# Kernel tuning notes

Measured on AMD Instinct MI355X. Metric: run time of the kernel, lower is better.

Reference implementation:

```python
import jax, jax.numpy as jnp
import numpy as np
import math

D_MODEL = 1024
N_HEADS = 16
HEAD_DIM = D_MODEL // N_HEADS


def rotate_half(x):
    x1, x2 = x[..., : x.shape[-1] // 2], x[..., x.shape[-1] // 2 :]
    return jnp.concatenate([-x2, x1], axis=-1)


def rope_cos_sin(T, dim, dtype):
    inv_freq = 1.0 / (10000.0 ** (jnp.arange(0, dim, 2, dtype=jnp.float32) / dim))
    t = jnp.arange(T, dtype=jnp.float32)
    freqs = jnp.einsum('i,j->ij', t, inv_freq)          # [T, dim/2]
    emb = jnp.concatenate([freqs, freqs], axis=-1)      # [T, dim]
    # broadcast shape [1, T, 1, dim] to match q/k of shape [B, T, H, dim]
    return emb.astype(dtype)[None, :, None, :]


def setup_inputs() -> dict:
    key = jax.random.key(0)
    k_x, k_qkv_w, k_qkv_b, k_p_w, k_p_b = jax.random.split(key, 5)
    B, T = 2, 2048
    s = 1.0 / math.sqrt(D_MODEL)
    return {
        'x': jax.random.normal(k_x, (B, T, D_MODEL), dtype=jnp.float32),
        'qkv_w': jax.random.uniform(k_qkv_w, (3 * D_MODEL, D_MODEL), minval=-s, maxval=s, dtype=jnp.float32),
        'qkv_b': jax.random.uniform(k_qkv_b, (3 * D_MODEL,), minval=-s, maxval=s, dtype=jnp.float32),
        'proj_w': jax.random.uniform(k_p_w, (D_MODEL, D_MODEL), minval=-s, maxval=s, dtype=jnp.float32),
        'proj_b': jax.random.uniform(k_p_b, (D_MODEL,), minval=-s, maxval=s, dtype=jnp.float32),
    }


def reference(x, qkv_w, qkv_b, proj_w, proj_b):
    B, T, C = x.shape
    H, Dh = N_HEADS, HEAD_DIM
    qkv = x @ qkv_w.T + qkv_b                           # [B, T, 3C]
    qkv = qkv.reshape(B, T, 3, H, Dh)
    q, k, v = qkv[:, :, 0], qkv[:, :, 1], qkv[:, :, 2]  # [B, T, H, Dh]
    emb = rope_cos_sin(T, Dh, x.dtype)
    cos, sin = jnp.cos(emb), jnp.sin(emb)
    q = q * cos + rotate_half(q) * sin
    k = k * cos + rotate_half(k) * sin
    # attention with causal mask (dropout in eval mode = identity)
    scale = 1.0 / math.sqrt(Dh)
    attn = jnp.einsum('bqhd,bkhd->bhqk', q, k) * scale  # [B, H, T, T]
    causal = jnp.tril(jnp.ones((T, T), dtype=bool))
    attn = jnp.where(causal, attn, -jnp.inf)
    attn = jax.nn.softmax(attn, axis=-1)
    out = jnp.einsum('bhqk,bkhd->bqhd', attn, v).reshape(B, T, C)
    return out @ proj_w.T + proj_b
```

## Files before the change

### kernel.cpp

```cpp
#include <hip/hip_runtime.h>
#include <math.h>

#define T_SEQ 2048
#define NB 2
#define NH 16
#define DH 64
#define DM 1024

typedef unsigned short u16;
typedef __attribute__((ext_vector_type(8))) __bf16 bf16x8;
typedef __attribute__((ext_vector_type(4))) __bf16 bf16v4;
typedef __attribute__((ext_vector_type(4))) short s16x4;
typedef __attribute__((ext_vector_type(4))) float f32x4;
typedef __attribute__((ext_vector_type(4))) int i32x4;

__device__ __forceinline__ u16 f2bf(float f) {
  return __builtin_bit_cast(u16, (__bf16)f);
}
__device__ __forceinline__ float bf2f(u16 v) {
  unsigned u = ((unsigned)v) << 16;
  return __builtin_bit_cast(float, u);
}
__device__ __forceinline__ bf16x8 ld_frag(const u16* p) {
  bf16x8 r; __builtin_memcpy(&r, p, 16); return r;
}
__device__ __forceinline__ s16x4 ld8(const u16* p) {
  s16x4 r; __builtin_memcpy(&r, p, 8); return r;
}
__device__ __forceinline__ i32x4 ld16(const u16* p) {
  i32x4 r; __builtin_memcpy(&r, p, 16); return r;
}
__device__ __forceinline__ void st16(u16* p, i32x4 v) {
  __builtin_memcpy(p, &v, 16);
}
__device__ __forceinline__ void cvt_store8(u16* dst, const float* src) {
  f32x4 a, b;
  __builtin_memcpy(&a, src, 16);
  __builtin_memcpy(&b, src + 4, 16);
  bf16x8 t;
  t[0] = (__bf16)a[0]; t[1] = (__bf16)a[1]; t[2] = (__bf16)a[2]; t[3] = (__bf16)a[3];
  t[4] = (__bf16)b[0]; t[5] = (__bf16)b[1]; t[6] = (__bf16)b[2]; t[7] = (__bf16)b[3];
  __builtin_memcpy(dst, &t, 16);
}
__device__ __forceinline__ void gld_lds16(const u16* g, u16* l) {
  __builtin_amdgcn_global_load_lds(
      (const __attribute__((address_space(1))) void*)g,
      (__attribute__((address_space(3))) void*)l, 16, 0, 0);
}

__global__ __launch_bounds__(256) void cvt_f32_bf16(const float* __restrict__ in,
                                                    u16* __restrict__ out, int n8) {
  const int i = blockIdx.x * 256 + threadIdx.x;
  if (i < n8) cvt_store8(out + (long)i * 8, in + (long)i * 8);
}

template <int MODE, int BN>
__global__ __launch_bounds__(256) void gemm_nt(
    const u16* __restrict__ A, const u16* __restrict__ Bw,
    const float* __restrict__ bias, float* __restrict__ out,
    u16* __restrict__ q_ws, u16* __restrict__ k_ws, u16* __restrict__ v_ws,
    int M, int N, int K) {
  constexpr int NTN = BN / 32;
  constexpr int WNS = BN / 2;
  __shared__ __align__(16) u16 As[128 * 32];
  __shared__ __align__(16) u16 Bs[BN * 32];
  const int tid = threadIdx.x;
  const int wave = tid >> 6, lane = tid & 63;
  const int quad = lane >> 4, l16 = lane & 15;
  const int wm = wave & 1, wn = wave >> 1;
  const int m0 = blockIdx.y * 128, n0 = blockIdx.x * BN;
  const int lrow = lane >> 2;
  const int lcol = (lane & 3) * 8;

  f32x4 acc[4][NTN] = {};

  const u16* Ag = A + (long)(m0 + wave * 16 + lrow) * K + lcol;
  const u16* Bg = Bw + (long)(n0 + wave * 16 + lrow) * K + lcol;
  u16* Al = &As[(wave * 16 + lrow) * 32 + lcol];
  u16* Bl = &Bs[(wave * 16 + lrow) * 32 + lcol];

  for (int k0 = 0; k0 < K; k0 += 32) {
    __syncthreads();
    gld_lds16(Ag + k0, Al);
    gld_lds16(Ag + (long)64 * K + k0, Al + 64 * 32);
    gld_lds16(Bg + k0, Bl);
    if constexpr (BN == 128) gld_lds16(Bg + (long)64 * K + k0, Bl + 64 * 32);
    __syncthreads();
    bf16x8 af[4], bfr[NTN];
#pragma unroll
    for (int mt = 0; mt < 4; mt++)
      af[mt] = ld_frag(&As[(wm * 64 + mt * 16 + l16) * 32 + quad * 8]);
#pragma unroll
    for (int nt = 0; nt < NTN; nt++)
      bfr[nt] = ld_frag(&Bs[(wn * WNS + nt * 16 + l16) * 32 + quad * 8]);
#pragma unroll
    for (int mt = 0; mt < 4; mt++)
#pragma unroll
      for (int nt = 0; nt < NTN; nt++)
        acc[mt][nt] = __builtin_amdgcn_mfma_f32_16x16x32_bf16(af[mt], bfr[nt],
                                                              acc[mt][nt], 0, 0, 0);
  }

  if constexpr (MODE == 1) {
#pragma unroll
    for (int nt = 0; nt < NTN; nt++) {
      const int col = n0 + wn * WNS + nt * 16 + l16;
      const float bv = bias[col];
#pragma unroll
      for (int mt = 0; mt < 4; mt++) {
        const int rbase = m0 + wm * 64 + mt * 16 + quad * 4;
#pragma unroll
        for (int r = 0; r < 4; r++)
          out[(long)(rbase + r) * N + col] = acc[mt][nt][r] + bv;
      }
    }
  } else {
    const int which = n0 >> 10;
#pragma unroll
    for (int np = 0; np < 2; np++) {
      const int col1 = n0 + wn * 64 + np * 16 + l16;
      const int rem = col1 & 1023;
      const int h = rem >> 6, dh = rem & 63;
      const float bv1 = bias[col1], bv2 = bias[col1 + 32];
      if (which == 2) {
#pragma unroll
        for (int mt = 0; mt < 4; mt++) {
          const int rbase = m0 + wm * 64 + mt * 16 + quad * 4;
          const int b = rbase >> 11;
#pragma unroll
          for (int r = 0; r < 4; r++) {
            const int t = (rbase + r) & (T_SEQ - 1);
            const long vb = (((long)(b * NH + h)) * DH) * T_SEQ + t;
            v_ws[vb + (long)dh * T_SEQ] = f2bf(acc[mt][np][r] + bv1);
            v_ws[vb + (long)(dh + 32) * T_SEQ] = f2bf(acc[mt][np + 2][r] + bv2);
          }
        }
      } else {
        const float invf = exp2f(-(float)dh * 0.41524101186092045f);
        const float cD = cosf(invf), sD = sinf(invf);
        u16* dst = (which == 0) ? q_ws : k_ws;
        const float sc = (which == 0) ? 0.125f : 1.0f;
#pragma unroll
        for (int mt = 0; mt < 4; mt++) {
          const int rbase = m0 + wm * 64 + mt * 16 + quad * 4;
          const int b = rbase >> 11;
          const int t0 = rbase & (T_SEQ - 1);
          float c = cosf((float)t0 * invf), s = sinf((float)t0 * invf);
#pragma unroll
          for (int r = 0; r < 4; r++) {
            const float v1 = acc[mt][np][r] + bv1;
            const float v2 = acc[mt][np + 2][r] + bv2;
            const float o1 = (v1 * c - v2 * s) * sc;
            const float o2 = (v2 * c + v1 * s) * sc;
            const long ib = (((long)(b * NH + h)) * T_SEQ + (t0 + r)) * DH;
            dst[ib + dh] = f2bf(o1);
            dst[ib + dh + 32] = f2bf(o2);
            const float cn = c * cD - s * sD;
            s = s * cD + c * sD;
            c = cn;
          }
        }
      }
    }
  }
}

__global__ __launch_bounds__(256, 4) void attn_kernel(const u16* __restrict__ q,
                                                      const u16* __restrict__ k,
                                                      const u16* __restrict__ v,
                                                      u16* __restrict__ o) {
  __shared__ __align__(16) u16 Ks[128 * 72];
  __shared__ __align__(16) u16 Vt[64 * 136];
  const int tid = threadIdx.x;
  const int wave = tid >> 6, lane = tid & 63;
  const int quad = lane >> 4, l16 = lane & 15;
  const int bh = blockIdx.x;
  const int y = blockIdx.y;
  const int kk = y >> 3, a = y & 7;
  const int qt = (kk == 0) ? (2 * a)
               : (kk == 1) ? (31 - 2 * a)
               : (kk == 2) ? (2 * a + 1)
                           : (30 - 2 * a);
  const long base = (long)bh * T_SEQ * DH;
  const int b = bh >> 4, h = bh & 15;

  const int q0 = qt * 64;
  const int qrow = q0 + wave * 16 + l16;
  bf16x8 bq0, bq1;
  {
    const u16* qr = q + base + (long)qrow * DH + quad * 8;
    bq0 = ld_frag(qr);
    bq1 = ld_frag(qr + 32);
  }
  float lst = 0.f;
  f32x4 oacc[4] = {};
  const int nkt = (q0 + 64 + 127) >> 7;

  const int k_rr = tid >> 3;
  const int k_cc = (tid & 7) * 8;
  const int v_d  = tid >> 4;
  const int v_cc = (tid & 15) * 8;
  const u16* kbase = k + base;
  const u16* vbase = v + base;

  i32x4 kreg[4], vreg[4];
#pragma unroll
  for (int p = 0; p < 4; p++) {
    kreg[p] = ld16(kbase + (long)(k_rr + p * 32) * DH + k_cc);
    vreg[p] = ld16(vbase + (long)(v_d + p * 16) * T_SEQ + v_cc);
  }
#pragma unroll
  for (int p = 0; p < 4; p++) {
    st16(&Ks[(k_rr + p * 32) * 72 + k_cc], kreg[p]);
    st16(&Vt[(v_d + p * 16) * 136 + v_cc], vreg[p]);
  }
  __syncthreads();

  for (int kt = 0; kt < nkt; kt++) {
    const int key0 = kt * 128;
    const bool last = (kt == nkt - 1);

    if (!last) {
      const int kn = key0 + 128;
#pragma unroll
      for (int p = 0; p < 4; p++) {
        kreg[p] = ld16(kbase + (long)kn * DH + (long)(k_rr + p * 32) * DH + k_cc);
        vreg[p] = ld16(vbase + kn + (long)(v_d + p * 16) * T_SEQ + v_cc);
      }
    }

#pragma unroll
    for (int hh = 0; hh < 2; hh++) {
      if (hh == 1 && last && key0 >= q0) continue;
      const int kb = key0 + hh * 64;

      f32x4 sfr[4];
#pragma unroll
      for (int nt = 0; nt < 4; nt++) {
        const int row = hh * 64 + nt * 16 + l16;
        bf16x8 k0f = ld_frag(&Ks[row * 72 + quad * 8]);
        bf16x8 k1f = ld_frag(&Ks[row * 72 + 32 + quad * 8]);
        f32x4 z = {0.f, 0.f, 0.f, 0.f};
        z = __builtin_amdgcn_mfma_f32_16x16x32_bf16(k0f, bq0, z, 0, 0, 0);
        z = __builtin_amdgcn_mfma_f32_16x16x32_bf16(k1f, bq1, z, 0, 0, 0);
        sfr[nt] = z;
      }

      if (last) {
#pragma unroll
        for (int nt = 0; nt < 4; nt++) {
          const int keyb = kb + nt * 16 + quad * 4;
#pragma unroll
          for (int r = 0; r < 4; r++)
            sfr[nt][r] = (keyb + r <= qrow) ? sfr[nt][r] : -1e30f;
        }
      }

      float rsum = 0.f;
      s16x4 pf[4];
#pragma unroll
      for (int nt = 0; nt < 4; nt++) {
        bf16v4 pv;
#pragma unroll
        for (int r = 0; r < 4; r++) {
          const float p =
              exp2f(__builtin_fmaf(sfr[nt][r], 1.44269504f, -46.166241f));
          rsum += p;
          pv[r] = (__bf16)p;
        }
        pf[nt] = __builtin_bit_cast(s16x4, pv);
      }
      rsum += __shfl_xor(rsum, 16, 64);
      rsum += __shfl_xor(rsum, 32, 64);
      lst += rsum;

#pragma unroll
      for (int ont = 0; ont < 4; ont++) {
        const u16* vrow = &Vt[(ont * 16 + l16) * 136 + hh * 64 + quad * 4];
#pragma unroll
        for (int nt = 0; nt < 4; nt++) {
          s16x4 vf = ld8(vrow + nt * 16);
          oacc[ont] = __builtin_amdgcn_mfma_f32_16x16x16bf16_1k(vf, pf[nt],
                                                                oacc[ont], 0, 0, 0);
        }
      }
    }

    if (!last) {
      __syncthreads();
#pragma unroll
      for (int p = 0; p < 4; p++) {
        st16(&Ks[(k_rr + p * 32) * 72 + k_cc], kreg[p]);
        st16(&Vt[(v_d + p * 16) * 136 + v_cc], vreg[p]);
      }
      __syncthreads();
    }
  }

  const float inv_l = 1.f / lst;
  u16* orow = o + ((long)(b * T_SEQ + qrow)) * DM + h * DH + quad * 4;
#pragma unroll
  for (int ont = 0; ont < 4; ont++) {
    bf16v4 t4;
#pragma unroll
    for (int r = 0; r < 4; r++) t4[r] = (__bf16)(oacc[ont][r] * inv_l);
    __builtin_memcpy(orow + ont * 16, &t4, 8);
  }
}

extern "C" void kernel_launch(void* const* d_in, const int* in_sizes, int n_in,
                              void* d_out, int out_size, void* d_ws, size_t ws_size,
                              hipStream_t stream) {
  const float* x      = (const float*)d_in[0];
  const float* qkv_w  = (const float*)d_in[1];
  const float* qkv_b  = (const float*)d_in[2];
  const float* proj_w = (const float*)d_in[3];
  const float* proj_b = (const float*)d_in[4];
  float* out = (float*)d_out;

  u16* ws = (u16*)d_ws;
  const long per = (long)NB * NH * T_SEQ * DH;
  u16* q_ws = ws;
  u16* k_ws = ws + per;
  u16* v_ws = ws + 2 * per;
  u16* ao_ws = ws + 3 * per;
  u16* x_bf  = ws + 3 * per;
  u16* w_bf  = ws + 4 * per;

  dim3 blk(256);
  cvt_f32_bf16<<<2048, blk, 0, stream>>>(x, x_bf, (int)(per / 8));
  cvt_f32_bf16<<<1536, blk, 0, stream>>>(qkv_w, w_bf, 3 * DM * DM / 8);
  gemm_nt<0, 128><<<dim3(24, 32), blk, 0, stream>>>(x_bf, w_bf, qkv_b, nullptr,
                                                    q_ws, k_ws, v_ws, 4096, 3072, 1024);
  attn_kernel<<<dim3(32, 32), blk, 0, stream>>>(q_ws, k_ws, v_ws, ao_ws);
  cvt_f32_bf16<<<512, blk, 0, stream>>>(proj_w, w_bf, DM * DM / 8);
  gemm_nt<1, 64><<<dim3(16, 32), blk, 0, stream>>>(ao_ws, w_bf, proj_b, out,
                                                   nullptr, nullptr, nullptr, 4096, 1024, 1024);
}
```

Before: 197.8 us.

## Load K and V fragments directly from global memory, dropping LDS staging

The attention kernel no longer stages K and V tiles in shared memory with register prefetch and block barriers. Each wave now loads its K and V MFMA fragments straight from global memory, one 64-key block at a time. This removes the LDS traffic and the __syncthreads calls. In exchange, every wave re-reads the same K/V data from global or cache, and the loads are narrower and less coalesced, with no software prefetch to hide their latency.

```diff
diff --git a/kernel.cpp b/kernel.cpp
--- a/kernel.cpp
+++ b/kernel.cpp
@@ -169,8 +169,6 @@
                                                       const u16* __restrict__ k,
                                                       const u16* __restrict__ v,
                                                       u16* __restrict__ o) {
-  __shared__ __align__(16) u16 Ks[128 * 72];
-  __shared__ __align__(16) u16 Vt[64 * 136];
   const int tid = threadIdx.x;
   const int wave = tid >> 6, lane = tid & 63;
   const int quad = lane >> 4, l16 = lane & 15;
@@ -194,106 +192,67 @@
   }
   float lst = 0.f;
   f32x4 oacc[4] = {};
-  const int nkt = (q0 + 64 + 127) >> 7;
-
-  const int k_rr = tid >> 3;
-  const int k_cc = (tid & 7) * 8;
-  const int v_d  = tid >> 4;
-  const int v_cc = (tid & 15) * 8;
   const u16* kbase = k + base;
   const u16* vbase = v + base;
 
-  i32x4 kreg[4], vreg[4];
-#pragma unroll
-  for (int p = 0; p < 4; p++) {
-    kreg[p] = ld16(kbase + (long)(k_rr + p * 32) * DH + k_cc);
-    vreg[p] = ld16(vbase + (long)(v_d + p * 16) * T_SEQ + v_cc);
-  }
-#pragma unroll
-  for (int p = 0; p < 4; p++) {
-    st16(&Ks[(k_rr + p * 32) * 72 + k_cc], kreg[p]);
-    st16(&Vt[(v_d + p * 16) * 136 + v_cc], vreg[p]);
-  }
-  __syncthreads();
-
-  for (int kt = 0; kt < nkt; kt++) {
-    const int key0 = kt * 128;
-    const bool last = (kt == nkt - 1);
-
-    if (!last) {
-      const int kn = key0 + 128;
-#pragma unroll
-      for (int p = 0; p < 4; p++) {
-        kreg[p] = ld16(kbase + (long)kn * DH + (long)(k_rr + p * 32) * DH + k_cc);
-        vreg[p] = ld16(vbase + kn + (long)(v_d + p * 16) * T_SEQ + v_cc);
-      }
-    }
-
-#pragma unroll
-    for (int hh = 0; hh < 2; hh++) {
-      if (hh == 1 && last && key0 >= q0) continue;
-      const int kb = key0 + hh * 64;
-
-      f32x4 sfr[4];
+  for (int sb = 0; sb <= qt; sb++) {
+    const int kb = sb * 64;
+    const bool last = (sb == qt);
+
+    bf16x8 kf0[4], kf1[4];
+#pragma unroll
+    for (int nt = 0; nt < 4; nt++) {
+      const u16* kr = kbase + (long)(kb + nt * 16 + l16) * DH + quad * 8;
+      kf0[nt] = ld_frag(kr);
+      kf1[nt] = ld_frag(kr + 32);
+    }
+
+    f32x4 sfr[4];
+#pragma unroll
+    for (int nt = 0; nt < 4; nt++) {
+      f32x4 z = {0.f, 0.f, 0.f, 0.f};
+      z = __builtin_amdgcn_mfma_f32_16x16x32_bf16(kf0[nt], bq0, z, 0, 0, 0);
+      z = __builtin_amdgcn_mfma_f32_16x16x32_bf16(kf1[nt], bq1, z, 0, 0, 0);
+      sfr[nt] = z;
+    }
+
+    if (last) {
 #pragma unroll
       for (int nt = 0; nt < 4; nt++) {
-        const int row = hh * 64 + nt * 16 + l16;
-        bf16x8 k0f = ld_frag(&Ks[row * 72 + quad * 8]);
-        bf16x8 k1f = ld_frag(&Ks[row * 72 + 32 + quad * 8]);
-        f32x4 z = {0.f, 0.f, 0.f, 0.f};
-        z = __builtin_amdgcn_mfma_f32_16x16x32_bf16(k0f, bq0, z, 0, 0, 0);
-        z = __builtin_amdgcn_mfma_f32_16x16x32_bf16(k1f, bq1, z, 0, 0, 0);
-        sfr[nt] = z;
-      }
-
-      if (last) {
-#pragma unroll
-        for (int nt = 0; nt < 4; nt++) {
-          const int keyb = kb + nt * 16 + quad * 4;
-#pragma unroll
-          for (int r = 0; r < 4; r++)
-            sfr[nt][r] = (keyb + r <= qrow) ? sfr[nt][r] : -1e30f;
-        }
-      }
-
-      float rsum = 0.f;
-      s16x4 pf[4];
+        const int keyb = kb + nt * 16 + quad * 4;
+#pragma unroll
+        for (int r = 0; r < 4; r++)
+          sfr[nt][r] = (keyb + r <= qrow) ? sfr[nt][r] : -1e30f;
+      }
+    }
+
+    float rsum = 0.f;
+    s16x4 pf[4];
+#pragma unroll
+    for (int nt = 0; nt < 4; nt++) {
+      bf16v4 pv;
+#pragma unroll
+      for (int r = 0; r < 4; r++) {
+        const float p =
+            exp2f(__builtin_fmaf(sfr[nt][r], 1.44269504f, -46.166241f));
+        rsum += p;
+        pv[r] = (__bf16)p;
+      }
+      pf[nt] = __builtin_bit_cast(s16x4, pv);
+    }
+    rsum += __shfl_xor(rsum, 16, 64);
+    rsum += __shfl_xor(rsum, 32, 64);
+    lst += rsum;
+
+#pragma unroll
+    for (int ont = 0; ont < 4; ont++) {
+      const u16* vrow = vbase + (long)(ont * 16 + l16) * T_SEQ + kb + quad * 4;
 #pragma unroll
       for (int nt = 0; nt < 4; nt++) {
-        bf16v4 pv;
-#pragma unroll
-        for (int r = 0; r < 4; r++) {
-          const float p =
-              exp2f(__builtin_fmaf(sfr[nt][r], 1.44269504f, -46.166241f));
-          rsum += p;
-          pv[r] = (__bf16)p;
-        }
-        pf[nt] = __builtin_bit_cast(s16x4, pv);
-      }
-      rsum += __shfl_xor(rsum, 16, 64);
-      rsum += __shfl_xor(rsum, 32, 64);
-      lst += rsum;
-
-#pragma unroll
-      for (int ont = 0; ont < 4; ont++) {
-        const u16* vrow = &Vt[(ont * 16 + l16) * 136 + hh * 64 + quad * 4];
-#pragma unroll
-        for (int nt = 0; nt < 4; nt++) {
-          s16x4 vf = ld8(vrow + nt * 16);
-          oacc[ont] = __builtin_amdgcn_mfma_f32_16x16x16bf16_1k(vf, pf[nt],
-                                                                oacc[ont], 0, 0, 0);
-        }
-      }
-    }
-
-    if (!last) {
-      __syncthreads();
-#pragma unroll
-      for (int p = 0; p < 4; p++) {
-        st16(&Ks[(k_rr + p * 32) * 72 + k_cc], kreg[p]);
-        st16(&Vt[(v_d + p * 16) * 136 + v_cc], vreg[p]);
-      }
-      __syncthreads();
+        s16x4 vf = ld8(vrow + nt * 16);
+        oacc[ont] = __builtin_amdgcn_mfma_f32_16x16x16bf16_1k(vf, pf[nt],
+                                                              oacc[ont], 0, 0, 0);
+      }
     }
   }
 
```

Result: slower. 324.0 us (+63.8%).
